# Performance work log

Measured on AMD Instinct MI355X. Metric: run time of the kernel, lower is better.

The kernel has to match this reference:

```python
import jax, jax.numpy as jnp
import numpy as np

D = 8   # data_dimensions = len(rbf_list) = ARD lengthscale length
I0 = 0  # evaluated_dimension

def setup_inputs() -> dict:
    key = jax.random.key(0)
    k1, k2, k3, k4 = jax.random.split(key, 4)
    x1 = jax.random.normal(k1, (1024, D), jnp.float32)
    x2 = jax.random.normal(k2, (1024, D), jnp.float32)
    # positive lengthscales/variances, as in a trained RBF kernel
    lengthscale = jax.random.uniform(k3, (D, D), jnp.float32, 0.5, 1.5)  # L[j,k]: kernel j, dim k
    sigma = jax.random.uniform(k4, (D,), jnp.float32, 0.5, 1.5)          # sigma_k of kernel j
    return {"x1": x1, "x2": x2, "lengthscale": lengthscale, "sigma": sigma}


def _j_equals_l(x1, x2, L, sigma):
    # desired diagonal (j == l) entries, shape [n, m, d]
    inv2 = 1.0 / L ** 2                                    # [d, d]
    diff2 = (x1[:, None, :] - x2[None, :, :]) ** 2          # [n, m, d]
    T2 = inv2[I0][None, :] + 2.0 * inv2                     # [l, k]
    exp_sum = jnp.exp(-0.5 * jnp.einsum('nmk,lk->nml', diff2, T2))
    l_il2 = L[I0] ** 2                                      # [d]
    tl = inv2[I0] + jnp.diagonal(inv2)                      # inv2[I0,l] + inv2[l,l]
    poly = (-diff2 * (5.0 * tl + l_il2 * tl ** 2)
            + tl ** 2 * diff2 ** 2 + 2.0 + l_il2 * tl)
    return sigma / l_il2 ** 2 * poly * exp_sum              # [n, m, d]


def reference(x1, x2, lengthscale, sigma):
    L = lengthscale
    inv2 = 1.0 / L ** 2                                     # [j, k]
    diff2 = (x1[:, None, :] - x2[None, :, :]) ** 2          # [n, m, k]
    # T[a, b, k] = inv2[I0,k] + inv2[a,k] + inv2[b,k]
    T = inv2[I0][None, None, :] + inv2[:, None, :] + inv2[None, :, :]
    exp_sum = jnp.exp(-0.5 * jnp.einsum('nmk,abk->nmab', diff2, T))  # [n,m,c,j]
    l_ij2 = L[I0] ** 2                                      # [d], indexed by j
    M = inv2[I0][:, None] + inv2.T                          # M[c,j] = inv2[I0,c] + inv2[j,c]
    outer = (sigma[None, :] / l_ij2[None, :] ** 2 * M ** 2
             * (1.0 / M - diff2[:, :, :, None])             # component l = c (dim 2)
             * (l_ij2[None, :] - diff2[:, :, None, :])      # component j   (dim 3)
             * exp_sum)                                     # [n, m, c, j]
    desired_diag = _j_equals_l(x1, x2, L, sigma)            # [n, m, d]
    current_diag = jnp.diagonal(outer, axis1=2, axis2=3)    # [n, m, d]
    eye = jnp.eye(D, dtype=outer.dtype)
    corrected = outer + (desired_diag - current_diag)[:, :, :, None] * eye
    inner = jnp.sum(corrected, axis=3)                      # [n, m, c]
    return sigma[I0] * jnp.sum(inner, axis=2)               # [n, m]
```

## Files before the change

### kernel.cpp

```cpp
#include <hip/hip_runtime.h>

#define DD 8
#define LOG2E_HALF 0.7213475204444817f

__global__ void setup_coeffs(const float* __restrict__ L,
                             const float* __restrict__ sigma,
                             float* __restrict__ cf) {
    int t = threadIdx.x;
    int j = t >> 3;
    int c = t & 7;

    float Ljc_ = L[j * DD + c];
    cf[j * DD + c] = LOG2E_HALF / (Ljc_ * Ljc_);

    float s0  = sigma[0];
    float L0j = L[j];
    float l2j = L0j * L0j;
    float sJ  = sigma[j] / (l2j * l2j);
    float L0c = L[c];
    float Ljc = L[j * DD + c];
    float Mcj = 1.0f / (L0c * L0c) + 1.0f / (Ljc * Ljc);
    float G   = s0 * sJ * Mcj;
    cf[64  + j * DD + c] = G;
    cf[128 + j * DD + c] = G * Mcj;

    if (t < DD) {
        int d = t;
        float L0d = L[d];
        float l2  = L0d * L0d;
        cf[192 + d] = l2;
        float Ldd = L[d * DD + d];
        float tl  = 1.0f / l2 + 1.0f / (Ldd * Ldd);
        float sd  = sigma[d] / (l2 * l2);
        cf[200 + d] = -4.0f * s0 * sd * tl;
        cf[208 + d] =  2.0f * s0 * sd;
    }
}

__global__ __launch_bounds__(256) void rbf_main(
        const float* __restrict__ x1, const float* __restrict__ x2,
        const float* __restrict__ cf, float* __restrict__ out,
        int N, int M) {
    int m = blockIdx.x * 256 + threadIdx.x;
    int n = blockIdx.y;
    if (m >= M) return;

    const float* xr = x1 + (size_t)n * DD;
    const float4 ya = *reinterpret_cast<const float4*>(x2 + (size_t)m * DD);
    const float4 yb = *reinterpret_cast<const float4*>(x2 + (size_t)m * DD + 4);
    float yv[DD] = {ya.x, ya.y, ya.z, ya.w, yb.x, yb.y, yb.z, yb.w};

    float dd[DD];
#pragma unroll
    for (int k = 0; k < DD; ++k) {
        float dif = xr[k] - yv[k];
        dd[k] = dif * dif;
    }

    float e[DD];
#pragma unroll
    for (int c = 0; c < DD; ++c) {
        float A = 0.0f;
#pragma unroll
        for (int k = 0; k < DD; ++k) A = fmaf(dd[k], cf[c * DD + k], A);
        e[c] = exp2f(-A);
    }

    float w[DD];
#pragma unroll
    for (int c = 0; c < DD; ++c) w[c] = dd[c] * e[c];

    float acc = 0.0f;
#pragma unroll
    for (int j = 0; j < DD; ++j) {
        float ge = 0.0f, kw = 0.0f;
#pragma unroll
        for (int c = 0; c < DD; ++c) {
            ge = fmaf(cf[64  + j * DD + c], e[c], ge);
            kw = fmaf(cf[128 + j * DD + c], w[c], kw);
        }
        float fj = (cf[192 + j] - dd[j]) * e[j];
        acc = fmaf(fj, ge - kw, acc);
    }

#pragma unroll
    for (int d = 0; d < DD; ++d) {
        float adj = fmaf(cf[200 + d], dd[d], cf[208 + d]);
        acc = fmaf(adj * e[d], e[d], acc);
    }

    out[(size_t)n * M + m] = e[0] * acc;
}

extern "C" void kernel_launch(void* const* d_in, const int* in_sizes, int n_in,
                              void* d_out, int out_size, void* d_ws, size_t ws_size,
                              hipStream_t stream) {
    const float* x1 = (const float*)d_in[0];
    const float* x2 = (const float*)d_in[1];
    const float* L  = (const float*)d_in[2];
    const float* sg = (const float*)d_in[3];
    float* out = (float*)d_out;
    float* cf  = (float*)d_ws;

    int N = in_sizes[0] / DD;
    int M = in_sizes[1] / DD;

    setup_coeffs<<<1, 64, 0, stream>>>(L, sg, cf);
    dim3 grid((M + 255) / 256, N);
    rbf_main<<<grid, 256, 0, stream>>>(x1, x2, cf, out, N, M);
}
```

Baseline: 69.81 us.

## Fuse coefficient setup into main kernel and process four columns per thread

Removes the separate setup launch: each block now computes the 216 coefficients into shared memory before doing its work. Each thread also handles four m columns, so coefficient loads are reused across them and the block count drops fourfold. With M=1024 the grid becomes 1 x N blocks, and each block redundantly recomputes the coefficients. Register pressure rises from the dd/e/w arrays of size 4x8.

```diff
diff --git a/kernel.cpp b/kernel.cpp
--- a/kernel.cpp
+++ b/kernel.cpp
@@ -1,95 +1,120 @@
 #include <hip/hip_runtime.h>
 
 #define DD 8
+#define MPT 4
 #define LOG2E_HALF 0.7213475204444817f
 
-__global__ void setup_coeffs(const float* __restrict__ L,
-                             const float* __restrict__ sigma,
-                             float* __restrict__ cf) {
-    int t = threadIdx.x;
-    int j = t >> 3;
-    int c = t & 7;
+__global__ __launch_bounds__(256) void rbf_fused(
+        const float* __restrict__ x1, const float* __restrict__ x2,
+        const float* __restrict__ L, const float* __restrict__ sigma,
+        float* __restrict__ out, int N, int M) {
+    __shared__ float cf[216];
+    const int t = threadIdx.x;
+    if (t < 64) {
+        const int j = t >> 3, c = t & 7;
+        float s0   = sigma[0];
+        float Ljc  = L[j * DD + c];
+        float i2jc = 1.0f / (Ljc * Ljc);
+        cf[j * DD + c] = LOG2E_HALF * i2jc;
+        float L0j = L[j];
+        float l2j = L0j * L0j;
+        float sJ  = sigma[j] / (l2j * l2j);
+        float L0c = L[c];
+        float Mcj = 1.0f / (L0c * L0c) + i2jc;
+        float G   = s0 * sJ * Mcj;
+        cf[64  + j * DD + c] = G;
+        cf[128 + j * DD + c] = G * Mcj;
+        if (t < DD) {
+            int d = t;
+            float L0d = L[d];
+            float l2  = L0d * L0d;
+            cf[192 + d] = l2;
+            float Ldd = L[d * DD + d];
+            float tl  = 1.0f / l2 + 1.0f / (Ldd * Ldd);
+            float sd  = sigma[d] / (l2 * l2);
+            cf[200 + d] = -4.0f * s0 * sd * tl;
+            cf[208 + d] =  2.0f * s0 * sd;
+        }
+    }
+    __syncthreads();
 
-    float Ljc_ = L[j * DD + c];
-    cf[j * DD + c] = LOG2E_HALF / (Ljc_ * Ljc_);
-
-    float s0  = sigma[0];
-    float L0j = L[j];
-    float l2j = L0j * L0j;
-    float sJ  = sigma[j] / (l2j * l2j);
-    float L0c = L[c];
-    float Ljc = L[j * DD + c];
-    float Mcj = 1.0f / (L0c * L0c) + 1.0f / (Ljc * Ljc);
-    float G   = s0 * sJ * Mcj;
-    cf[64  + j * DD + c] = G;
-    cf[128 + j * DD + c] = G * Mcj;
-
-    if (t < DD) {
-        int d = t;
-        float L0d = L[d];
-        float l2  = L0d * L0d;
-        cf[192 + d] = l2;
-        float Ldd = L[d * DD + d];
-        float tl  = 1.0f / l2 + 1.0f / (Ldd * Ldd);
-        float sd  = sigma[d] / (l2 * l2);
-        cf[200 + d] = -4.0f * s0 * sd * tl;
-        cf[208 + d] =  2.0f * s0 * sd;
-    }
-}
-
-__global__ __launch_bounds__(256) void rbf_main(
-        const float* __restrict__ x1, const float* __restrict__ x2,
-        const float* __restrict__ cf, float* __restrict__ out,
-        int N, int M) {
-    int m = blockIdx.x * 256 + threadIdx.x;
-    int n = blockIdx.y;
-    if (m >= M) return;
+    const int n  = blockIdx.y;
+    const int m0 = blockIdx.x * (MPT * 256);
 
     const float* xr = x1 + (size_t)n * DD;
-    const float4 ya = *reinterpret_cast<const float4*>(x2 + (size_t)m * DD);
-    const float4 yb = *reinterpret_cast<const float4*>(x2 + (size_t)m * DD + 4);
-    float yv[DD] = {ya.x, ya.y, ya.z, ya.w, yb.x, yb.y, yb.z, yb.w};
+    float xv[DD];
+#pragma unroll
+    for (int k = 0; k < DD; ++k) xv[k] = xr[k];
 
-    float dd[DD];
+    float dd[MPT][DD], e[MPT][DD], w[MPT][DD];
 #pragma unroll
-    for (int k = 0; k < DD; ++k) {
-        float dif = xr[k] - yv[k];
-        dd[k] = dif * dif;
+    for (int q = 0; q < MPT; ++q) {
+        int m = m0 + t + q * 256;
+        int mc = m < M ? m : M - 1;
+        const float4 ya = *reinterpret_cast<const float4*>(x2 + (size_t)mc * DD);
+        const float4 yb = *reinterpret_cast<const float4*>(x2 + (size_t)mc * DD + 4);
+        float yv[DD] = {ya.x, ya.y, ya.z, ya.w, yb.x, yb.y, yb.z, yb.w};
+#pragma unroll
+        for (int k = 0; k < DD; ++k) {
+            float dif = xv[k] - yv[k];
+            dd[q][k] = dif * dif;
+        }
     }
 
-    float e[DD];
 #pragma unroll
     for (int c = 0; c < DD; ++c) {
-        float A = 0.0f;
+        float bc[DD];
 #pragma unroll
-        for (int k = 0; k < DD; ++k) A = fmaf(dd[k], cf[c * DD + k], A);
-        e[c] = exp2f(-A);
+        for (int k = 0; k < DD; ++k) bc[k] = cf[c * DD + k];
+#pragma unroll
+        for (int q = 0; q < MPT; ++q) {
+            float A = 0.0f;
+#pragma unroll
+            for (int k = 0; k < DD; ++k) A = fmaf(dd[q][k], bc[k], A);
+            float ec = exp2f(-A);
+            e[q][c] = ec;
+            w[q][c] = dd[q][c] * ec;
+        }
     }
 
-    float w[DD];
-#pragma unroll
-    for (int c = 0; c < DD; ++c) w[c] = dd[c] * e[c];
-
-    float acc = 0.0f;
+    float acc[MPT] = {0.0f, 0.0f, 0.0f, 0.0f};
 #pragma unroll
     for (int j = 0; j < DD; ++j) {
-        float ge = 0.0f, kw = 0.0f;
+        float gr[DD], kr[DD];
 #pragma unroll
         for (int c = 0; c < DD; ++c) {
-            ge = fmaf(cf[64  + j * DD + c], e[c], ge);
-            kw = fmaf(cf[128 + j * DD + c], w[c], kw);
+            gr[c] = cf[64  + j * DD + c];
+            kr[c] = cf[128 + j * DD + c];
         }
-        float fj = (cf[192 + j] - dd[j]) * e[j];
-        acc = fmaf(fj, ge - kw, acc);
+        float l2 = cf[192 + j];
+#pragma unroll
+        for (int q = 0; q < MPT; ++q) {
+            float ge = 0.0f, kw = 0.0f;
+#pragma unroll
+            for (int c = 0; c < DD; ++c) {
+                ge = fmaf(gr[c], e[q][c], ge);
+                kw = fmaf(kr[c], w[q][c], kw);
+            }
+            float fj = (l2 - dd[q][j]) * e[q][j];
+            acc[q] = fmaf(fj, ge - kw, acc[q]);
+        }
     }
 
 #pragma unroll
     for (int d = 0; d < DD; ++d) {
-        float adj = fmaf(cf[200 + d], dd[d], cf[208 + d]);
-        acc = fmaf(adj * e[d], e[d], acc);
+        float r1 = cf[200 + d], r0 = cf[208 + d];
+#pragma unroll
+        for (int q = 0; q < MPT; ++q) {
+            float adj = fmaf(r1, dd[q][d], r0);
+            acc[q] = fmaf(adj * e[q][d], e[q][d], acc[q]);
+        }
     }
 
-    out[(size_t)n * M + m] = e[0] * acc;
+#pragma unroll
+    for (int q = 0; q < MPT; ++q) {
+        int m = m0 + t + q * 256;
+        if (m < M) out[(size_t)n * M + m] = e[q][0] * acc[q];
+    }
 }
 
 extern "C" void kernel_launch(void* const* d_in, const int* in_sizes, int n_in,
@@ -100,12 +125,10 @@
     const float* L  = (const float*)d_in[2];
     const float* sg = (const float*)d_in[3];
     float* out = (float*)d_out;
-    float* cf  = (float*)d_ws;
 
     int N = in_sizes[0] / DD;
     int M = in_sizes[1] / DD;
 
-    setup_coeffs<<<1, 64, 0, stream>>>(L, sg, cf);
-    dim3 grid((M + 255) / 256, N);
-    rbf_main<<<grid, 256, 0, stream>>>(x1, x2, cf, out, N, M);
+    dim3 grid((M + MPT * 256 - 1) / (MPT * 256), N);
+    rbf_fused<<<grid, 256, 0, stream>>>(x1, x2, L, sg, out, N, M);
 }
```

After: 74.62 us. 1.07x slower.
